# Optimization experiments

Measured on AMD Instinct MI355X. Metric: run time of the kernel, lower is better.

Reference implementation:

```python
import jax, jax.numpy as jnp
import numpy as np

LEAKY_ALPHA = 0.2  # tf.nn.leaky_relu default

N_NODES = 65536
N_EDGES = 1048576
D = 64


def setup_inputs() -> dict:
    key = jax.random.key(0)
    k1, k2, k3, k4 = jax.random.split(key, 4)
    x = jax.random.normal(k1, (N_NODES, D), dtype=jnp.float32)
    edge_index = jax.random.randint(k2, (2, N_EDGES), 0, N_NODES, dtype=jnp.int64)
    W1 = jax.random.normal(k3, (D, D), dtype=jnp.float32) * 0.05
    b1 = jnp.zeros((D,), dtype=jnp.float32)
    W2 = jax.random.normal(k4, (D, D), dtype=jnp.float32) * 0.05
    b2 = jnp.zeros((D,), dtype=jnp.float32)
    return {"x": x, "edge_index": edge_index, "W1": W1, "b1": b1, "W2": W2, "b2": b2}


def _leaky_relu(v):
    return jnp.where(v >= 0, v, LEAKY_ALPHA * v)


def reference(x, edge_index, W1, b1, W2, b2):
    n = x.shape[0]
    src = edge_index[0]
    dst = edge_index[1]
    # LightGCN symmetric normalization: w_e = deg[src]^-1/2 * deg[dst]^-1/2
    ones = jnp.ones(src.shape, dtype=x.dtype)
    deg = jax.ops.segment_sum(ones, dst, num_segments=n)
    inv_sqrt = jnp.where(deg > 0, jax.lax.rsqrt(jnp.maximum(deg, 1.0)), 0.0)
    w = inv_sqrt[src] * inv_sqrt[dst]  # [E]
    # SpMM: h = normed_adj @ x  (gather + weighted scatter-add)
    h = jax.ops.segment_sum(x[src] * w[:, None], dst, num_segments=n)  # [N, D]
    # dual dense transform + elementwise gate
    out = _leaky_relu(h @ W1 + b1) + _leaky_relu((x * h) @ W2 + b2)
    return out
```

## Files before the change

### kernel.cpp

```cpp
#include <hip/hip_runtime.h>

#define N_NODES 65536
#define N_EDGES 1048576
#define D 64
#define NB 256
#define CHUNK (N_EDGES / NB)
#define SSTAGE 6144
#define FBCAP 65536

typedef __bf16 bf16x8 __attribute__((ext_vector_type(8)));
typedef float f32x4 __attribute__((ext_vector_type(4)));

__device__ __forceinline__ int edge_at(const void* ei, int is64, long long pos) {
    if (is64) return (int)((const long long*)ei)[pos];
    return ((const int*)ei)[pos];
}

__device__ __forceinline__ int detect_is64(const unsigned* ei, int* s_is64) {
    if (threadIdx.x < 64) {
        unsigned v = ei[2 * threadIdx.x + 1];
        unsigned long long nz = __ballot(v != 0u);
        if (threadIdx.x == 0) *s_is64 = (nz == 0ull) ? 1 : 0;
    }
    __syncthreads();
    return *s_is64;
}

__global__ __launch_bounds__(256) void passA_kernel(const void* ei,
                                                    unsigned* __restrict__ H,
                                                    unsigned* __restrict__ L,
                                                    unsigned* __restrict__ pairs_cs) {
    __shared__ unsigned ed[CHUNK];
    __shared__ unsigned srt[CHUNK];
    __shared__ unsigned hist[NB];
    __shared__ unsigned scn[NB];
    __shared__ int s_is64;
    const int is64 = detect_is64((const unsigned*)ei, &s_is64);
    const int t = threadIdx.x;
    const int w = blockIdx.x;
    hist[t] = 0;
    __syncthreads();
    const int base = w * CHUNK;
    for (int i = t; i < CHUNK; i += 256) {
        unsigned src = (unsigned)edge_at(ei, is64, base + i);
        unsigned dst = (unsigned)edge_at(ei, is64, (long long)N_EDGES + base + i);
        ed[i] = src | (dst << 16);
        atomicAdd(&hist[dst >> 8], 1u);
    }
    __syncthreads();
    const unsigned own = hist[t];
    scn[t] = own;
    __syncthreads();
    for (int off = 1; off < NB; off <<= 1) {
        unsigned v = (t >= off) ? scn[t - off] : 0u;
        __syncthreads();
        scn[t] += v;
        __syncthreads();
    }
    const unsigned excl = scn[t] - own;
    H[t * NB + w] = own;
    L[t * NB + w] = excl;
    hist[t] = excl;
    __syncthreads();
    for (int i = t; i < CHUNK; i += 256) {
        unsigned p = ed[i];
        unsigned pos = atomicAdd(&hist[p >> 24], 1u);
        srt[pos] = p;
    }
    __syncthreads();
    for (int i = t; i < CHUNK; i += 256) pairs_cs[(size_t)w * CHUNK + i] = srt[i];
}

__global__ __launch_bounds__(256) void bucketB_kernel(const unsigned* __restrict__ pairs_cs,
                                                      const unsigned* __restrict__ H,
                                                      const unsigned* __restrict__ L,
                                                      const float* __restrict__ x,
                                                      unsigned* __restrict__ row_start,
                                                      unsigned short* __restrict__ src16,
                                                      unsigned* __restrict__ y32,
                                                      unsigned* __restrict__ fb) {
    __shared__ unsigned s_pairs[SSTAGE];
    __shared__ unsigned short s_src[SSTAGE];
    __shared__ unsigned hist[NB];
    __shared__ unsigned scn[NB];
    __shared__ unsigned degs[NB];
    __shared__ unsigned s_tot[NB];
    const int t = threadIdx.x;
    const int b = blockIdx.x;

    {
        const uint4* Hr = (const uint4*)(H + t * NB);
        unsigned tt = 0;
#pragma unroll 8
        for (int k = 0; k < NB / 4; ++k) {
            uint4 q = Hr[k];
            tt += q.x + q.y + q.z + q.w;
        }
        s_tot[t] = tt;
        scn[t] = tt;
    }
    __syncthreads();
    for (int off = 1; off < NB; off <<= 1) {
        unsigned v = (t >= off) ? scn[t - off] : 0u;
        __syncthreads();
        scn[t] += v;
        __syncthreads();
    }
    const unsigned base = scn[b] - s_tot[b];
    const unsigned cnt = s_tot[b];
    const bool staged = (cnt <= SSTAGE);
    __syncthreads();

    const unsigned Hb = H[b * NB + t];
    const unsigned Lb = L[b * NB + t];
    scn[t] = Hb;
    __syncthreads();
    for (int off = 1; off < NB; off <<= 1) {
        unsigned v = (t >= off) ? scn[t - off] : 0u;
        __syncthreads();
        scn[t] += v;
        __syncthreads();
    }
    const unsigned ex = scn[t] - Hb;
    unsigned* wp = staged ? s_pairs : (fb + (size_t)b * FBCAP);
    for (unsigned j = 0; j < Hb; ++j) wp[ex + j] = pairs_cs[(size_t)t * CHUNK + Lb + j];
    __syncthreads();
    const unsigned* pp = staged ? s_pairs : (fb + (size_t)b * FBCAP);

    hist[t] = 0;
    __syncthreads();
    for (unsigned i = t; i < cnt; i += 256u) {
        atomicAdd(&hist[(pp[i] >> 16) & 255u], 1u);
    }
    __syncthreads();
    const unsigned own = hist[t];
    degs[t] = own;
    scn[t] = own;
    __syncthreads();
    for (int off = 1; off < NB; off <<= 1) {
        unsigned v = (t >= off) ? scn[t - off] : 0u;
        __syncthreads();
        scn[t] += v;
        __syncthreads();
    }
    const unsigned excl = scn[t] - own;
    row_start[b * NB + t] = base + excl;
    if (b == NB - 1 && t == 0) row_start[N_NODES] = N_EDGES;
    hist[t] = excl;
    __syncthreads();
    if (staged) {
        for (unsigned i = t; i < cnt; i += 256u) {
            unsigned p = pp[i];
            unsigned pos = atomicAdd(&hist[(p >> 16) & 255u], 1u);
            s_src[pos] = (unsigned short)(p & 0xFFFFu);
        }
        __syncthreads();
        for (unsigned i = t; i < cnt; i += 256u) src16[base + i] = s_src[i];
    } else {
        for (unsigned i = t; i < cnt; i += 256u) {
            unsigned p = pp[i];
            unsigned pos = atomicAdd(&hist[(p >> 16) & 255u], 1u);
            src16[base + pos] = (unsigned short)(p & 0xFFFFu);
        }
    }
    const int nbase = b * NB;
    for (int idx = t; idx < NB * 32; idx += 256) {
        int nl = idx >> 5;
        int col = idx & 31;
        unsigned d = degs[nl];
        float w = d ? rsqrtf((float)d) : 0.f;
        float2 v = *(const float2*)(x + (nbase + nl) * D + col * 2);
        unsigned lo = (unsigned)__builtin_bit_cast(unsigned short, (__bf16)(v.x * w));
        unsigned hi = (unsigned)__builtin_bit_cast(unsigned short, (__bf16)(v.y * w));
        y32[(size_t)(nbase + nl) * 32 + col] = lo | (hi << 16);
    }
}

#define BLO(u) __uint_as_float((u) << 16)
#define BHI(u) __uint_as_float((u) & 0xffff0000u)
__device__ __forceinline__ unsigned pkbf(float lo, float hi) {
    return (unsigned)__builtin_bit_cast(unsigned short, (__bf16)lo) |
           ((unsigned)__builtin_bit_cast(unsigned short, (__bf16)hi) << 16);
}
__global__ __launch_bounds__(256) void spmm_kernel(const unsigned short* __restrict__ src16,
                                                   const unsigned* __restrict__ row_start,
                                                   const uint4* __restrict__ y128,
                                                   uint4* __restrict__ hb4) {
    const int lane = threadIdx.x & 63;
    const int grp = lane >> 3;
    const int r8 = lane & 7;
    int wid = (blockIdx.x * blockDim.x + threadIdx.x) >> 6;
    int nw = (gridDim.x * blockDim.x) >> 6;
    for (int n = wid; n < N_NODES; n += nw) {
        const unsigned start = row_start[n];
        const unsigned end = row_start[n + 1];
        float a0 = 0.f, a1 = 0.f, a2 = 0.f, a3 = 0.f;
        float a4 = 0.f, a5 = 0.f, a6 = 0.f, a7 = 0.f;
        float c0 = 0.f, c1 = 0.f, c2 = 0.f, c3 = 0.f;
        float c4 = 0.f, c5 = 0.f, c6 = 0.f, c7 = 0.f;
        for (unsigned i = start; i < end; i += 16u) {
            const unsigned e1 = end - 1u;
            const unsigned iA = i + grp;
            const unsigned iB = i + 8u + grp;
            int sA = (int)src16[iA < end ? iA : e1];
            int sB = (int)src16[iB < end ? iB : e1];
            uint4 pA = y128[sA * 8 + r8];
            uint4 pB = y128[sB * 8 + r8];
            if (iA < end) {
                a0 += BLO(pA.x); a1 += BHI(pA.x);
                a2 += BLO(pA.y); a3 += BHI(pA.y);
                a4 += BLO(pA.z); a5 += BHI(pA.z);
                a6 += BLO(pA.w); a7 += BHI(pA.w);
            }
            if (iB < end) {
                c0 += BLO(pB.x); c1 += BHI(pB.x);
                c2 += BLO(pB.y); c3 += BHI(pB.y);
                c4 += BLO(pB.z); c5 += BHI(pB.z);
                c6 += BLO(pB.w); c7 += BHI(pB.w);
            }
        }
        a0 += c0; a1 += c1; a2 += c2; a3 += c3;
        a4 += c4; a5 += c5; a6 += c6; a7 += c7;
        a0 += __shfl_xor(a0, 8); a0 += __shfl_xor(a0, 16); a0 += __shfl_xor(a0, 32);
        a1 += __shfl_xor(a1, 8); a1 += __shfl_xor(a1, 16); a1 += __shfl_xor(a1, 32);
        a2 += __shfl_xor(a2, 8); a2 += __shfl_xor(a2, 16); a2 += __shfl_xor(a2, 32);
        a3 += __shfl_xor(a3, 8); a3 += __shfl_xor(a3, 16); a3 += __shfl_xor(a3, 32);
        a4 += __shfl_xor(a4, 8); a4 += __shfl_xor(a4, 16); a4 += __shfl_xor(a4, 32);
        a5 += __shfl_xor(a5, 8); a5 += __shfl_xor(a5, 16); a5 += __shfl_xor(a5, 32);
        a6 += __shfl_xor(a6, 8); a6 += __shfl_xor(a6, 16); a6 += __shfl_xor(a6, 32);
        a7 += __shfl_xor(a7, 8); a7 += __shfl_xor(a7, 16); a7 += __shfl_xor(a7, 32);
        const float w = (end > start) ? rsqrtf((float)(end - start)) : 0.f;
        if (grp == 0) {
            uint4 v;
            v.x = pkbf(a0 * w, a1 * w);
            v.y = pkbf(a2 * w, a3 * w);
            v.z = pkbf(a4 * w, a5 * w);
            v.w = pkbf(a6 * w, a7 * w);
            hb4[(size_t)n * 8 + r8] = v;
        }
    }
}

__global__ __launch_bounds__(256) void dense_mfma_kernel(const float* __restrict__ x,
                                                         const uint4* __restrict__ hb4,
                                                         const float* __restrict__ W1,
                                                         const float* __restrict__ b1,
                                                         const float* __restrict__ W2,
                                                         const float* __restrict__ b2,
                                                         float* __restrict__ out) {
    const int lane = threadIdx.x & 63;
    const int lo = lane & 15;
    const int hi = lane >> 4;

    bf16x8 bw1[2][4], bw2[2][4];
#pragma unroll
    for (int kt = 0; kt < 2; ++kt)
#pragma unroll
        for (int nt = 0; nt < 4; ++nt) {
            bf16x8 v1, v2;
#pragma unroll
            for (int j = 0; j < 8; ++j) {
                int k = kt * 32 + hi * 8 + j;
                int n = nt * 16 + lo;
                v1[j] = (__bf16)W1[k * D + n];
                v2[j] = (__bf16)W2[k * D + n];
            }
            bw1[kt][nt] = v1;
            bw2[kt][nt] = v2;
        }
    float bb1[4], bb2[4];
#pragma unroll
    for (int nt = 0; nt < 4; ++nt) {
        bb1[nt] = b1[nt * 16 + lo];
        bb2[nt] = b2[nt * 16 + lo];
    }

    int wid = (blockIdx.x * blockDim.x + threadIdx.x) >> 6;
    int nw = (gridDim.x * blockDim.x) >> 6;
    for (int blk = wid; blk < N_NODES / 16; blk += nw) {
        const int rb = blk * 16;
        const uint4* hrow = hb4 + (size_t)(rb + lo) * 8;
        const float* xrow = x + (rb + lo) * D;
        bf16x8 ah[2], ag[2];
#pragma unroll
        for (int kt = 0; kt < 2; ++kt) {
            const int c = kt * 32 + hi * 8;
            uint4 hp = hrow[kt * 4 + hi];
            float4 xv0 = *(const float4*)(xrow + c);
            float4 xv1 = *(const float4*)(xrow + c + 4);
            ah[kt] = __builtin_bit_cast(bf16x8, hp);
            bf16x8 g;
            g[0] = (__bf16)(BLO(hp.x) * xv0.x);
            g[1] = (__bf16)(BHI(hp.x) * xv0.y);
            g[2] = (__bf16)(BLO(hp.y) * xv0.z);
            g[3] = (__bf16)(BHI(hp.y) * xv0.w);
            g[4] = (__bf16)(BLO(hp.z) * xv1.x);
            g[5] = (__bf16)(BHI(hp.z) * xv1.y);
            g[6] = (__bf16)(BLO(hp.w) * xv1.z);
            g[7] = (__bf16)(BHI(hp.w) * xv1.w);
            ag[kt] = g;
        }
        f32x4 acc1[4], acc2[4];
#pragma unroll
        for (int nt = 0; nt < 4; ++nt) {
            acc1[nt] = (f32x4){0.f, 0.f, 0.f, 0.f};
            acc2[nt] = (f32x4){0.f, 0.f, 0.f, 0.f};
        }
#pragma unroll
        for (int kt = 0; kt < 2; ++kt)
#pragma unroll
            for (int nt = 0; nt < 4; ++nt) {
                acc1[nt] = __builtin_amdgcn_mfma_f32_16x16x32_bf16(ah[kt], bw1[kt][nt], acc1[nt], 0, 0, 0);
                acc2[nt] = __builtin_amdgcn_mfma_f32_16x16x32_bf16(ag[kt], bw2[kt][nt], acc2[nt], 0, 0, 0);
            }
#pragma unroll
        for (int nt = 0; nt < 4; ++nt)
#pragma unroll
            for (int r = 0; r < 4; ++r) {
                float a1 = acc1[nt][r] + bb1[nt];
                float a2 = acc2[nt][r] + bb2[nt];
                a1 = (a1 >= 0.f) ? a1 : 0.2f * a1;
                a2 = (a2 >= 0.f) ? a2 : 0.2f * a2;
                out[(rb + hi * 4 + r) * D + nt * 16 + lo] = a1 + a2;
            }
    }
}

extern "C" void kernel_launch(void* const* d_in, const int* in_sizes, int n_in,
                              void* d_out, int out_size, void* d_ws, size_t ws_size,
                              hipStream_t stream) {
    const float* x  = (const float*)d_in[0];
    const void*  ei = d_in[1];
    const float* W1 = (const float*)d_in[2];
    const float* b1 = (const float*)d_in[3];
    const float* W2 = (const float*)d_in[4];
    const float* b2 = (const float*)d_in[5];
    float* out = (float*)d_out;

    char* p = (char*)d_ws;
    unsigned* row_start    = (unsigned*)p;       p += 266240;
    unsigned* H            = (unsigned*)p;       p += NB * NB * 4;
    unsigned* L            = (unsigned*)p;       p += NB * NB * 4;
    unsigned short* src16  = (unsigned short*)p; p += (size_t)N_EDGES * 2;
    unsigned* y32          = (unsigned*)p;       p += (size_t)N_NODES * 32 * 4;
    unsigned* hb           = (unsigned*)p;       p += (size_t)N_NODES * 32 * 4;
    unsigned* fb           = (unsigned*)p;

    unsigned* pairs_cs = (unsigned*)d_out;

    passA_kernel<<<NB, 256, 0, stream>>>(ei, H, L, pairs_cs);
    bucketB_kernel<<<NB, 256, 0, stream>>>(pairs_cs, H, L, x, row_start, src16, y32, fb);
    spmm_kernel<<<4096, 256, 0, stream>>>(src16, row_start, (const uint4*)y32, (uint4*)hb);
    dense_mfma_kernel<<<1024, 256, 0, stream>>>(x, (const uint4*)hb, W1, b1, W2, b2, out);
}
```

Before: 82.20 us.

## Map 8 nodes per wavefront in SpMM, one 8-lane group per node

New measurement: 72.71 us. 1.13x faster.

```diff
diff --git a/kernel.cpp b/kernel.cpp
--- a/kernel.cpp
+++ b/kernel.cpp
@@ -182,62 +182,51 @@
     return (unsigned)__builtin_bit_cast(unsigned short, (__bf16)lo) |
            ((unsigned)__builtin_bit_cast(unsigned short, (__bf16)hi) << 16);
 }
+__device__ __forceinline__ void acc8(uint4 p, float* a) {
+    a[0] += BLO(p.x); a[1] += BHI(p.x);
+    a[2] += BLO(p.y); a[3] += BHI(p.y);
+    a[4] += BLO(p.z); a[5] += BHI(p.z);
+    a[6] += BLO(p.w); a[7] += BHI(p.w);
+}
 __global__ __launch_bounds__(256) void spmm_kernel(const unsigned short* __restrict__ src16,
                                                    const unsigned* __restrict__ row_start,
                                                    const uint4* __restrict__ y128,
                                                    uint4* __restrict__ hb4) {
     const int lane = threadIdx.x & 63;
-    const int grp = lane >> 3;
+    const int g = lane >> 3;
     const int r8 = lane & 7;
-    int wid = (blockIdx.x * blockDim.x + threadIdx.x) >> 6;
-    int nw = (gridDim.x * blockDim.x) >> 6;
-    for (int n = wid; n < N_NODES; n += nw) {
+    int wv = (blockIdx.x * blockDim.x + threadIdx.x) >> 6;
+    int nwv = (gridDim.x * blockDim.x) >> 6;
+    for (int nb = wv * 8; nb < N_NODES; nb += nwv * 8) {
+        const int n = nb + g;
         const unsigned start = row_start[n];
         const unsigned end = row_start[n + 1];
-        float a0 = 0.f, a1 = 0.f, a2 = 0.f, a3 = 0.f;
-        float a4 = 0.f, a5 = 0.f, a6 = 0.f, a7 = 0.f;
-        float c0 = 0.f, c1 = 0.f, c2 = 0.f, c3 = 0.f;
-        float c4 = 0.f, c5 = 0.f, c6 = 0.f, c7 = 0.f;
-        for (unsigned i = start; i < end; i += 16u) {
-            const unsigned e1 = end - 1u;
-            const unsigned iA = i + grp;
-            const unsigned iB = i + 8u + grp;
-            int sA = (int)src16[iA < end ? iA : e1];
-            int sB = (int)src16[iB < end ? iB : e1];
-            uint4 pA = y128[sA * 8 + r8];
-            uint4 pB = y128[sB * 8 + r8];
-            if (iA < end) {
-                a0 += BLO(pA.x); a1 += BHI(pA.x);
-                a2 += BLO(pA.y); a3 += BHI(pA.y);
-                a4 += BLO(pA.z); a5 += BHI(pA.z);
-                a6 += BLO(pA.w); a7 += BHI(pA.w);
-            }
-            if (iB < end) {
-                c0 += BLO(pB.x); c1 += BHI(pB.x);
-                c2 += BLO(pB.y); c3 += BHI(pB.y);
-                c4 += BLO(pB.z); c5 += BHI(pB.z);
-                c6 += BLO(pB.w); c7 += BHI(pB.w);
-            }
-        }
-        a0 += c0; a1 += c1; a2 += c2; a3 += c3;
-        a4 += c4; a5 += c5; a6 += c6; a7 += c7;
-        a0 += __shfl_xor(a0, 8); a0 += __shfl_xor(a0, 16); a0 += __shfl_xor(a0, 32);
-        a1 += __shfl_xor(a1, 8); a1 += __shfl_xor(a1, 16); a1 += __shfl_xor(a1, 32);
-        a2 += __shfl_xor(a2, 8); a2 += __shfl_xor(a2, 16); a2 += __shfl_xor(a2, 32);
-        a3 += __shfl_xor(a3, 8); a3 += __shfl_xor(a3, 16); a3 += __shfl_xor(a3, 32);
-        a4 += __shfl_xor(a4, 8); a4 += __shfl_xor(a4, 16); a4 += __shfl_xor(a4, 32);
-        a5 += __shfl_xor(a5, 8); a5 += __shfl_xor(a5, 16); a5 += __shfl_xor(a5, 32);
-        a6 += __shfl_xor(a6, 8); a6 += __shfl_xor(a6, 16); a6 += __shfl_xor(a6, 32);
-        a7 += __shfl_xor(a7, 8); a7 += __shfl_xor(a7, 16); a7 += __shfl_xor(a7, 32);
+        float a[8] = {0.f, 0.f, 0.f, 0.f, 0.f, 0.f, 0.f, 0.f};
+        float c[8] = {0.f, 0.f, 0.f, 0.f, 0.f, 0.f, 0.f, 0.f};
+        unsigned i = start;
+        for (; i + 4 <= end; i += 4) {
+            int s0 = (int)src16[i];
+            int s1 = (int)src16[i + 1];
+            int s2 = (int)src16[i + 2];
+            int s3 = (int)src16[i + 3];
+            uint4 p0 = y128[s0 * 8 + r8];
+            uint4 p1 = y128[s1 * 8 + r8];
+            uint4 p2 = y128[s2 * 8 + r8];
+            uint4 p3 = y128[s3 * 8 + r8];
+            acc8(p0, a); acc8(p1, c);
+            acc8(p2, a); acc8(p3, c);
+        }
+        for (; i < end; ++i) {
+            uint4 p = y128[(int)src16[i] * 8 + r8];
+            acc8(p, a);
+        }
         const float w = (end > start) ? rsqrtf((float)(end - start)) : 0.f;
-        if (grp == 0) {
-            uint4 v;
-            v.x = pkbf(a0 * w, a1 * w);
-            v.y = pkbf(a2 * w, a3 * w);
-            v.z = pkbf(a4 * w, a5 * w);
-            v.w = pkbf(a6 * w, a7 * w);
-            hb4[(size_t)n * 8 + r8] = v;
-        }
+        uint4 v;
+        v.x = pkbf((a[0] + c[0]) * w, (a[1] + c[1]) * w);
+        v.y = pkbf((a[2] + c[2]) * w, (a[3] + c[3]) * w);
+        v.z = pkbf((a[4] + c[4]) * w, (a[5] + c[5]) * w);
+        v.w = pkbf((a[6] + c[6]) * w, (a[7] + c[7]) * w);
+        hb4[(size_t)nb * 8 + lane] = v;
     }
 }
 
@@ -350,6 +339,6 @@
 
     passA_kernel<<<NB, 256, 0, stream>>>(ei, H, L, pairs_cs);
     bucketB_kernel<<<NB, 256, 0, stream>>>(pairs_cs, H, L, x, row_start, src16, y32, fb);
-    spmm_kernel<<<4096, 256, 0, stream>>>(src16, row_start, (const uint4*)y32, (uint4*)hb);
+    spmm_kernel<<<2048, 256, 0, stream>>>(src16, row_start, (const uint4*)y32, (uint4*)hb);
     dense_mfma_kernel<<<1024, 256, 0, stream>>>(x, (const uint4*)hb, W1, b1, W2, b2, out);
 }
```
